# Kernel tuning notes

Hardware: AMD Instinct MI355X
Metric: run time of the kernel (lower is better)

## Reference

```python
import jax, jax.numpy as jnp
import numpy as np

DIM = 512
HEADS = 8
HEAD_DIM = DIM // HEADS
SCALE = HEAD_DIM ** -0.5
LN_EPS = 1e-5


def _layernorm(t, g, b):
    mu = jnp.mean(t, axis=-1, keepdims=True)
    var = jnp.mean(jnp.square(t - mu), axis=-1, keepdims=True)
    return (t - mu) * jax.lax.rsqrt(var + LN_EPS) * g + b


def setup_inputs() -> dict:
    key = jax.random.key(0)
    ks = jax.random.split(key, 8)
    B, C, H, W = 2, DIM, 48, 48
    s = 1.0 / np.sqrt(DIM)
    return {
        "x": jax.random.normal(ks[0], (B, C, H, W), jnp.float32),
        "y": jax.random.normal(ks[1], (B, C, H, W), jnp.float32),
        # linear weights stored [in, out]
        "k_w": jax.random.uniform(ks[2], (DIM, DIM), jnp.float32, -s, s),
        "k_b": jax.random.uniform(ks[3], (DIM,), jnp.float32, -s, s),
        "qv_w": jax.random.uniform(ks[4], (DIM, 2 * DIM), jnp.float32, -s, s),
        "qv_b": jax.random.uniform(ks[5], (2 * DIM,), jnp.float32, -s, s),
        "lnx_g": jnp.ones((DIM,), jnp.float32),
        "lnx_b": jnp.zeros((DIM,), jnp.float32),
        "lny_g": jnp.ones((DIM,), jnp.float32),
        "lny_b": jnp.zeros((DIM,), jnp.float32),
    }


def _split_qv(t, qv_w, qv_b):
    B, N, C = t.shape
    qv = (t @ qv_w + qv_b).reshape(B, N, 2, HEADS, HEAD_DIM)
    qv = jnp.transpose(qv, (2, 0, 3, 1, 4))  # [2, B, h, N, d]
    return qv[0], qv[1]


def _heads(t):
    B, N, C = t.shape
    return jnp.transpose(t.reshape(B, N, HEADS, HEAD_DIM), (0, 2, 1, 3))  # [B,h,N,d]


def reference(x, y, k_w, k_b, qv_w, qv_b, lnx_g, lnx_b, lny_g, lny_b):
    B, C = x.shape[0], x.shape[1]
    xf = _layernorm(jnp.transpose(x.reshape(B, C, -1), (0, 2, 1)), lnx_g, lnx_b)  # [B,N,C]
    yf = _layernorm(jnp.transpose(y.reshape(B, C, -1), (0, 2, 1)), lny_g, lny_b)
    N = xf.shape[1]

    y_q, y_v = _split_qv(yf, qv_w, qv_b)
    x_q, x_v = _split_qv(xf, qv_w, qv_b)
    y_k = _heads(yf @ k_w + k_b)
    x_k = _heads(xf @ k_w + k_b)

    # branch 1: softmax(x_q y_k^T) x_v  -> standard [B,N,C]
    a1 = jax.nn.softmax(jnp.einsum('bhnd,bhmd->bhnm', x_q, y_k) * SCALE, axis=-1)
    xo = jnp.einsum('bhnm,bhmd->bhnd', a1, x_v)
    xo = jnp.transpose(xo, (0, 2, 1, 3)).reshape(B, N, C)

    # branch 2: faithful reproduction of torch quirk (x_k kept a leading 1-dim,
    # so the output [1,B,h,N,d].transpose(1,2).reshape(B,N,C) scrambles layout)
    a2 = jax.nn.softmax(jnp.einsum('bhnd,bhmd->bhnm', y_q, x_k) * SCALE, axis=-1)
    yo = jnp.einsum('bhnm,bhmd->bhnd', a2, y_v)  # [B,h,N,d]
    yo = jnp.transpose(yo[None], (0, 2, 1, 3, 4)).reshape(B, N, C)

    return jnp.concatenate([xo, yo], axis=0)  # [2B, N, C]
```

## Files before the change

### kernel.cpp

```cpp
#include <hip/hip_runtime.h>

#define DIM 512
#define NTOK 2304
#define HEADS 8
#define HD 64
#define LN_EPS 1e-5f
#define BNC 2359296
#define QSC 0.18033688011112042f

typedef __attribute__((ext_vector_type(8))) short short8;
typedef __attribute__((ext_vector_type(4))) short sh4;
typedef __attribute__((ext_vector_type(4))) float f32x4;

__device__ __forceinline__ short f2bf(float f) {
    union { float f; unsigned u; } x; x.f = f;
    unsigned r = (x.u + 0x7fffu + ((x.u >> 16) & 1u)) >> 16;
    return (short)(r & 0xffffu);
}
__device__ __forceinline__ unsigned fbits(float f) {
    union { float f; unsigned u; } x; x.f = f; return x.u;
}
__device__ __forceinline__ void gl2lds(const short* g, short* l) {
    __builtin_amdgcn_global_load_lds(
        (const __attribute__((address_space(1))) unsigned int*)g,
        (__attribute__((address_space(3))) unsigned int*)l, 16, 0, 0);
}

__global__ void k_pre(const float* __restrict__ x, const float* __restrict__ y,
                      const float* __restrict__ qv_w, const float* __restrict__ k_w,
                      const float* __restrict__ qv_b, const float* __restrict__ k_b,
                      const float* __restrict__ gx, const float* __restrict__ bx,
                      const float* __restrict__ gy, const float* __restrict__ by,
                      short* __restrict__ T, short* __restrict__ Wt,
                      float* __restrict__ bias) {
    __shared__ __align__(16) float tile[64][65];
    __shared__ float pS[4][64], pQ[4][64];
    __shared__ float muL[64], rsL[64];
    int bkid = blockIdx.x, tid = threadIdx.x;
    if (bkid < 1152) {
        int nt = bkid % 36, ct = (bkid / 36) % 8, sb = bkid / 288;
        int s = sb >> 1, b = sb & 1;
        int n0 = nt * 64, c0 = ct * 64;
        const float* src = (s ? y : x) + (size_t)b * DIM * NTOK;
        int nl = tid & 63, part = tid >> 6;
        {
            const float* p = src + n0 + nl;
            float sum = 0.f, sq = 0.f;
            for (int c = part * 128; c < part * 128 + 128; c++) {
                float v = p[(size_t)c * NTOK];
                sum += v; sq += v * v;
            }
            pS[part][nl] = sum; pQ[part][nl] = sq;
        }
        __syncthreads();
        if (tid < 64) {
            float ts = pS[0][tid] + pS[1][tid] + pS[2][tid] + pS[3][tid];
            float tq = pQ[0][tid] + pQ[1][tid] + pQ[2][tid] + pQ[3][tid];
            float m = ts * (1.0f / DIM);
            float var = tq * (1.0f / DIM) - m * m;
            muL[tid] = m;
            rsL[tid] = rsqrtf(var + LN_EPS);
        }
        for (int slot = tid; slot < 1024; slot += 256) {
            int r = slot >> 4, q = slot & 15;
            const float* p = src + (size_t)(c0 + r) * NTOK + n0 + q * 4;
            float4 v = *(const float4*)p;
            tile[r][q*4+0] = v.x; tile[r][q*4+1] = v.y;
            tile[r][q*4+2] = v.z; tile[r][q*4+3] = v.w;
        }
        __syncthreads();
        const float* g  = s ? gy : gx;
        const float* be = s ? by : bx;
        int nr = tid >> 2, cg = tid & 3;
        float m = muL[nr], r_ = rsL[nr];
        short8 o0, o1;
        for (int i = 0; i < 8; i++) {
            int c = c0 + cg * 16 + i;
            o0[i] = f2bf((tile[cg*16+i][nr] - m) * r_ * g[c] + be[c]);
        }
        for (int i = 0; i < 8; i++) {
            int c = c0 + cg * 16 + 8 + i;
            o1[i] = f2bf((tile[cg*16+8+i][nr] - m) * r_ * g[c] + be[c]);
        }
        short* dst = T + ((size_t)sb * NTOK + n0 + nr) * DIM + c0 + cg * 16;
        *(short8*)dst = o0;
        *(short8*)(dst + 8) = o1;
        return;
    }
    int idx = bkid - 1152;
    int jt = idx % 24, ct = idx / 24;
    int j0 = jt * 64, c0 = ct * 64;
    if (ct == 0 && tid < 64) {
        int j = j0 + tid;
        bias[j] = (j < 1024) ? qv_b[j] : k_b[j - 1024];
    }
    for (int slot = tid; slot < 1024; slot += 256) {
        int r = slot >> 4, q = slot & 15;
        int c = c0 + r;
        float4 v;
        if (j0 < 1024) v = *(const float4*)(qv_w + (size_t)c * 1024 + j0 + q * 4);
        else           v = *(const float4*)(k_w  + (size_t)c * 512  + (j0 - 1024) + q * 4);
        tile[r][q*4+0] = v.x; tile[r][q*4+1] = v.y;
        tile[r][q*4+2] = v.z; tile[r][q*4+3] = v.w;
    }
    __syncthreads();
    int jr = tid >> 2, cg = tid & 3;
    short8 o0, o1;
    for (int i = 0; i < 8; i++) o0[i] = f2bf(tile[cg*16+i][jr]);
    for (int i = 0; i < 8; i++) o1[i] = f2bf(tile[cg*16+8+i][jr]);
    short* dst = Wt + (size_t)(j0 + jr) * DIM + c0 + cg * 16;
    *(short8*)dst = o0;
    *(short8*)(dst + 8) = o1;
}

__global__ void __launch_bounds__(256)
k_gemm(const short* __restrict__ T, const short* __restrict__ Wt,
       const float* __restrict__ bias, short* __restrict__ QVK,
       short* __restrict__ VT) {
    __shared__ __align__(16) short smem[2 * 128 * 64];
    short* As = smem;
    short* Bs = smem + 128 * 64;
    int n0 = blockIdx.x * 128, j0 = blockIdx.y * 128, sb = blockIdx.z;
    int tid = threadIdx.x;
    int w = tid >> 6, l = tid & 63;
    int wr = w >> 1, wc = w & 1;
    int lrow = l & 15, quad = l >> 4;
    int r_in = (l >> 3) & 7, cc = l & 7;
    int ch = cc ^ r_in;
    int sw0 = (quad ^ (lrow & 7)) * 8;
    const short* Ab = T + (size_t)sb * NTOK * DIM;
    f32x4 acc[4][4] = {};
    for (int kk = 0; kk < 8; kk++) {
        if (kk) __syncthreads();
        for (int inst = 0; inst < 4; inst++) {
            int R = w * 32 + inst * 8 + r_in;
            gl2lds(Ab + (size_t)(n0 + R) * 512 + kk * 64 + ch * 8,
                   &As[(w * 32 + inst * 8) * 64]);
            gl2lds(Wt + (size_t)(j0 + R) * 512 + kk * 64 + ch * 8,
                   &Bs[(w * 32 + inst * 8) * 64]);
        }
        __syncthreads();
        for (int c2 = 0; c2 < 2; c2++) {
            int off = c2 ? (sw0 ^ 32) : sw0;
            short8 af[4], bf[4];
            for (int i = 0; i < 4; i++)
                af[i] = *(const short8*)&As[(wr*64 + i*16 + lrow) * 64 + off];
            for (int j = 0; j < 4; j++)
                bf[j] = *(const short8*)&Bs[(wc*64 + j*16 + lrow) * 64 + off];
            for (int i = 0; i < 4; i++)
                for (int j = 0; j < 4; j++)
                    acc[i][j] = __builtin_amdgcn_mfma_f32_16x16x32_bf16(af[i], bf[j], acc[i][j], 0, 0, 0);
        }
    }
    if (j0 >= 512 && j0 < 1024) {
        __syncthreads();
        for (int i = 0; i < 4; i++)
            for (int j = 0; j < 4; j++) {
                int jloc = wc * 64 + j * 16 + lrow;
                float bv = bias[j0 + jloc];
                int nloc = wr * 64 + i * 16 + quad * 4;
                int c8 = nloc >> 3, half = (nloc >> 2) & 1;
                sh4 pk;
                for (int reg = 0; reg < 4; reg++) pk[reg] = f2bf(acc[i][j][reg] + bv);
                *(sh4*)&smem[jloc * 128 + ((c8 ^ (jloc & 15)) * 8) + half * 4] = pk;
            }
        __syncthreads();
        for (int slot = tid; slot < 2048; slot += 256) {
            int row = slot >> 4, seg = slot & 15;
            short8 v = *(const short8*)&smem[row * 128 + ((seg ^ (row & 15)) * 8)];
            *(short8*)(VT + ((size_t)sb * 512 + (j0 - 512) + row) * NTOK + n0 + seg * 8) = v;
        }
    } else {
        for (int i = 0; i < 4; i++)
            for (int j = 0; j < 4; j++) {
                int jj = j0 + wc * 64 + j * 16 + lrow;
                float bv = bias[jj];
                float sc = (jj < 512) ? QSC : 1.0f;
                for (int reg = 0; reg < 4; reg++) {
                    int n = n0 + wr * 64 + i * 16 + quad * 4 + reg;
                    QVK[((size_t)sb * NTOK + n) * 1536 + jj] = f2bf((acc[i][j][reg] + bv) * sc);
                }
            }
    }
}

__global__ void __launch_bounds__(256)
k_attn(const short* __restrict__ QVK, const short* __restrict__ VT,
       float* __restrict__ out, float* __restrict__ O1,
       float* __restrict__ l0, float* __restrict__ l1) {
    __shared__ __align__(16) short Ks[64 * 64];
    __shared__ __align__(16) short Vs[64 * 64];
    __shared__ __align__(16) short Qs[64 * 64];
    int id = blockIdx.x;
    int half = id / 1152;
    int rid = id % 1152;
    int xcd = rid & 7, rem = rid >> 3;
    int qt = rem % 36, yhi = rem / 36;
    int yb = yhi * 8 + xcd;
    int br = yb >> 4;
    int b  = (yb >> 3) & 1;
    int h  = yb & 7;
    int tid = threadIdx.x;
    int w = tid >> 6, l = tid & 63;
    int lrow = l & 15, quad = l >> 4;
    int r_in = (l >> 3) & 7, cc = l & 7;
    int ch = cc ^ r_in;
    int sw0 = (quad ^ (lrow & 7)) * 8;
    int n0 = qt * 64;
    int m_base = half * 1152;
    const short* Qg = QVK + ((size_t)(br * 2 + b) * NTOK) * 1536 + h * 64;
    const short* Kg = QVK + ((size_t)((1 - br) * 2 + b) * NTOK) * 1536 + 1024 + h * 64;
    const short* Vg = VT + ((size_t)(br * 2 + b) * 512 + h * 64) * NTOK;

    for (int inst = 0; inst < 2; inst++) {
        int R = w * 16 + inst * 8 + r_in;
        gl2lds(Qg + (size_t)(n0 + R) * 1536 + ch * 8, &Qs[(w * 16 + inst * 8) * 64]);
    }

    const short* KgA = Kg + (size_t)(m_base + w * 16 + r_in) * 1536 + ch * 8;
    const short* KgB = Kg + (size_t)(m_base + w * 16 + 8 + r_in) * 1536 + ch * 8;
    const short* VgA = Vg + (size_t)(w * 16 + r_in) * NTOK + m_base + ch * 8;
    const short* VgB = Vg + (size_t)(w * 16 + 8 + r_in) * NTOK + m_base + ch * 8;
    int lds_off = l * 8;

    short8 ka = *(const short8*)(KgA);
    short8 kb = *(const short8*)(KgB);
    short8 va = *(const short8*)(VgA);
    short8 vb = *(const short8*)(VgB);
    const short* Kc = KgA + (size_t)64 * 1536;
    const short* Kd = KgB + (size_t)64 * 1536;
    const short* Vc = VgA + 64;
    const short* Vd = VgB + 64;

    __syncthreads();
    short8 bq0 = *(const short8*)&Qs[(w * 16 + lrow) * 64 + sw0];
    short8 bq1 = *(const short8*)&Qs[(w * 16 + lrow) * 64 + (sw0 ^ 32)];
    short* Pw = &Qs[w * 16 * 64];

    short8 ones;
    for (int i = 0; i < 8; i++) ones[i] = (short)0x3F80;

    f32x4 Oacc[4] = {};
    f32x4 lacc = {};

    for (int mt = 0; mt < 18; mt++) {
        __syncthreads();
        *(short8*)&Ks[(w * 16)     * 64 + lds_off] = ka;
        *(short8*)&Ks[(w * 16 + 8) * 64 + lds_off] = kb;
        *(short8*)&Vs[(w * 16)     * 64 + lds_off] = va;
        *(short8*)&Vs[(w * 16 + 8) * 64 + lds_off] = vb;
        __syncthreads();
        if (mt + 1 < 18) {
            ka = *(const short8*)(Kc);
            kb = *(const short8*)(Kd);
            va = *(const short8*)(Vc);
            vb = *(const short8*)(Vd);
        }
        Kc += (size_t)64 * 1536;
        Kd += (size_t)64 * 1536;
        Vc += 64;
        Vd += 64;
        __builtin_amdgcn_sched_barrier(0);

        for (int sub = 0; sub < 4; sub++) {
            short8 ak0 = *(const short8*)&Ks[(sub * 16 + lrow) * 64 + sw0];
            short8 ak1 = *(const short8*)&Ks[(sub * 16 + lrow) * 64 + (sw0 ^ 32)];
            f32x4 a = {};
            a = __builtin_amdgcn_mfma_f32_16x16x32_bf16(ak0, bq0, a, 0, 0, 0);
            a = __builtin_amdgcn_mfma_f32_16x16x32_bf16(ak1, bq1, a, 0, 0, 0);
            float p0 = exp2f(a[0]), p1 = exp2f(a[1]);
            float p2 = exp2f(a[2]), p3 = exp2f(a[3]);
            uint2 pk;
            pk.x = __builtin_amdgcn_perm(fbits(p1), fbits(p0), 0x07060302u);
            pk.y = __builtin_amdgcn_perm(fbits(p3), fbits(p2), 0x07060302u);
            *(uint2*)&Pw[lrow * 64 + (((2 * sub + (quad >> 1)) ^ (lrow & 7)) * 8) + (quad & 1) * 4] = pk;
        }

        short8 ap0 = *(const short8*)&Pw[lrow * 64 + sw0];
        short8 ap1 = *(const short8*)&Pw[lrow * 64 + (sw0 ^ 32)];
        lacc = __builtin_amdgcn_mfma_f32_16x16x32_bf16(ones, ap0, lacc, 0, 0, 0);
        lacc = __builtin_amdgcn_mfma_f32_16x16x32_bf16(ones, ap1, lacc, 0, 0, 0);
        for (int ddt = 0; ddt < 4; ddt++) {
            short8 av0 = *(const short8*)&Vs[(ddt * 16 + lrow) * 64 + sw0];
            short8 av1 = *(const short8*)&Vs[(ddt * 16 + lrow) * 64 + (sw0 ^ 32)];
            Oacc[ddt] = __builtin_amdgcn_mfma_f32_16x16x32_bf16(av0, ap0, Oacc[ddt], 0, 0, 0);
            Oacc[ddt] = __builtin_amdgcn_mfma_f32_16x16x32_bf16(av1, ap1, Oacc[ddt], 0, 0, 0);
        }
    }

    int n = n0 + w * 16 + lrow;
    if (quad == 0) (half ? l1 : l0)[yb * NTOK + n] = lacc[0];
    for (int ddt = 0; ddt < 4; ddt++) {
        float4 o;
        o.x = Oacc[ddt][0];
        o.y = Oacc[ddt][1];
        o.z = Oacc[ddt][2];
        o.w = Oacc[ddt][3];
        if (half == 0) {
            if (br == 0)
                *(float4*)&out[((size_t)b * NTOK + n) * 512 + h * 64 + ddt * 16 + quad * 4] = o;
            else
                *(float4*)&out[(size_t)BNC + ((size_t)(h * 2 + b) * NTOK + n) * 64 + ddt * 16 + quad * 4] = o;
        } else {
            *(float4*)&O1[((size_t)yb * NTOK + n) * 64 + ddt * 16 + quad * 4] = o;
        }
    }
}

__global__ void __launch_bounds__(256)
k_norm(float* __restrict__ out, const float* __restrict__ O1,
       const float* __restrict__ l0, const float* __restrict__ l1) {
    int i = blockIdx.x * 256 + threadIdx.x;
    int o = i * 4;
    int yb, n, d;
    if (o < BNC) {
        int b = o / (NTOK * 512);
        int r = o % (NTOK * 512);
        n = r >> 9;
        int c = r & 511;
        d = c & 63;
        yb = b * 8 + (c >> 6);
    } else {
        int o2 = o - BNC;
        int hb = o2 / (NTOK * 64);
        n = (o2 >> 6) % NTOK;
        d = o2 & 63;
        yb = 16 + (hb & 1) * 8 + (hb >> 1);
    }
    int li = yb * NTOK + n;
    float linv = 1.f / (l0[li] + l1[li]);
    float4 a = *(const float4*)&out[o];
    float4 q = *(const float4*)&O1[(size_t)li * 64 + d];
    a.x = (a.x + q.x) * linv;
    a.y = (a.y + q.y) * linv;
    a.z = (a.z + q.z) * linv;
    a.w = (a.w + q.w) * linv;
    *(float4*)&out[o] = a;
}

extern "C" void kernel_launch(void* const* d_in, const int* in_sizes, int n_in,
                              void* d_out, int out_size, void* d_ws, size_t ws_size,
                              hipStream_t stream) {
    const float* x     = (const float*)d_in[0];
    const float* y     = (const float*)d_in[1];
    const float* k_w   = (const float*)d_in[2];
    const float* k_b   = (const float*)d_in[3];
    const float* qv_w  = (const float*)d_in[4];
    const float* qv_b  = (const float*)d_in[5];
    const float* lnx_g = (const float*)d_in[6];
    const float* lnx_b = (const float*)d_in[7];
    const float* lny_g = (const float*)d_in[8];
    const float* lny_b = (const float*)d_in[9];
    float* out = (float*)d_out;

    char* ws = (char*)d_ws;
    float* bias = (float*)ws;
    short* T    = (short*)(ws + 6144);
    short* Wt   = T + 4718592;
    short* QVK  = Wt + 786432;
    short* VT   = QVK + 14155776;
    float* O1   = (float*)(ws + 48764928);
    float* l0   = (float*)(ws + 67639296);
    float* l1   = (float*)(ws + 67934208);

    k_pre  <<<1344, 256, 0, stream>>>(x, y, qv_w, k_w, qv_b, k_b,
                                      lnx_g, lnx_b, lny_g, lny_b, T, Wt, bias);
    k_gemm <<<dim3(18, 12, 4), 256, 0, stream>>>(T, Wt, bias, QVK, VT);
    k_attn <<<2304, 256, 0, stream>>>(QVK, VT, out, O1, l0, l1);
    k_norm <<<4608, 256, 0, stream>>>(out, O1, l0, l1);
}
```

Baseline: 202.3 us.

## Double-buffer K/V tiles in LDS and use native exp2 intrinsic

Splits the K and V shared-memory tiles into two buffers so that the next tile is written to LDS after the current tile's MFMA work, leaving one barrier per iteration instead of two. Global loads are issued two tiles ahead in registers. exp2f is also replaced with the hardware exp2 builtin to skip range handling. This costs double the LDS for K/V, which may lower occupancy. The native exp2 may also differ for denormal or edge inputs.

```diff
diff --git a/kernel.cpp b/kernel.cpp
--- a/kernel.cpp
+++ b/kernel.cpp
@@ -188,8 +188,8 @@
 k_attn(const short* __restrict__ QVK, const short* __restrict__ VT,
        float* __restrict__ out, float* __restrict__ O1,
        float* __restrict__ l0, float* __restrict__ l1) {
-    __shared__ __align__(16) short Ks[64 * 64];
-    __shared__ __align__(16) short Vs[64 * 64];
+    __shared__ __align__(16) short Kbuf[2][64 * 64];
+    __shared__ __align__(16) short Vbuf[2][64 * 64];
     __shared__ __align__(16) short Qs[64 * 64];
     int id = blockIdx.x;
     int half = id / 1152;
@@ -217,50 +217,46 @@
         gl2lds(Qg + (size_t)(n0 + R) * 1536 + ch * 8, &Qs[(w * 16 + inst * 8) * 64]);
     }
 
-    const short* KgA = Kg + (size_t)(m_base + w * 16 + r_in) * 1536 + ch * 8;
-    const short* KgB = Kg + (size_t)(m_base + w * 16 + 8 + r_in) * 1536 + ch * 8;
-    const short* VgA = Vg + (size_t)(w * 16 + r_in) * NTOK + m_base + ch * 8;
-    const short* VgB = Vg + (size_t)(w * 16 + 8 + r_in) * NTOK + m_base + ch * 8;
+    const short* KnA = Kg + (size_t)(m_base + w * 16 + r_in) * 1536 + ch * 8;
+    const short* KnB = Kg + (size_t)(m_base + w * 16 + 8 + r_in) * 1536 + ch * 8;
+    const short* VnA = Vg + (size_t)(w * 16 + r_in) * NTOK + m_base + ch * 8;
+    const short* VnB = Vg + (size_t)(w * 16 + 8 + r_in) * NTOK + m_base + ch * 8;
     int lds_off = l * 8;
 
-    short8 ka = *(const short8*)(KgA);
-    short8 kb = *(const short8*)(KgB);
-    short8 va = *(const short8*)(VgA);
-    short8 vb = *(const short8*)(VgB);
-    const short* Kc = KgA + (size_t)64 * 1536;
-    const short* Kd = KgB + (size_t)64 * 1536;
-    const short* Vc = VgA + 64;
-    const short* Vd = VgB + 64;
+    short8 ka = *(const short8*)(KnA);
+    short8 kb = *(const short8*)(KnB);
+    short8 va = *(const short8*)(VnA);
+    short8 vb = *(const short8*)(VnB);
+    KnA += (size_t)64 * 1536; KnB += (size_t)64 * 1536;
+    VnA += 64; VnB += 64;
 
     __syncthreads();
     short8 bq0 = *(const short8*)&Qs[(w * 16 + lrow) * 64 + sw0];
     short8 bq1 = *(const short8*)&Qs[(w * 16 + lrow) * 64 + (sw0 ^ 32)];
     short* Pw = &Qs[w * 16 * 64];
 
+    *(short8*)&Kbuf[0][(w * 16)     * 64 + lds_off] = ka;
+    *(short8*)&Kbuf[0][(w * 16 + 8) * 64 + lds_off] = kb;
+    *(short8*)&Vbuf[0][(w * 16)     * 64 + lds_off] = va;
+    *(short8*)&Vbuf[0][(w * 16 + 8) * 64 + lds_off] = vb;
+    ka = *(const short8*)(KnA);
+    kb = *(const short8*)(KnB);
+    va = *(const short8*)(VnA);
+    vb = *(const short8*)(VnB);
+    KnA += (size_t)64 * 1536; KnB += (size_t)64 * 1536;
+    VnA += 64; VnB += 64;
+
     short8 ones;
     for (int i = 0; i < 8; i++) ones[i] = (short)0x3F80;
 
     f32x4 Oacc[4] = {};
     f32x4 lacc = {};
+    int cur = 0;
 
     for (int mt = 0; mt < 18; mt++) {
         __syncthreads();
-        *(short8*)&Ks[(w * 16)     * 64 + lds_off] = ka;
-        *(short8*)&Ks[(w * 16 + 8) * 64 + lds_off] = kb;
-        *(short8*)&Vs[(w * 16)     * 64 + lds_off] = va;
-        *(short8*)&Vs[(w * 16 + 8) * 64 + lds_off] = vb;
-        __syncthreads();
-        if (mt + 1 < 18) {
-            ka = *(const short8*)(Kc);
-            kb = *(const short8*)(Kd);
-            va = *(const short8*)(Vc);
-            vb = *(const short8*)(Vd);
-        }
-        Kc += (size_t)64 * 1536;
-        Kd += (size_t)64 * 1536;
-        Vc += 64;
-        Vd += 64;
-        __builtin_amdgcn_sched_barrier(0);
+        const short* Ks = Kbuf[cur];
+        const short* Vs = Vbuf[cur];
 
         for (int sub = 0; sub < 4; sub++) {
             short8 ak0 = *(const short8*)&Ks[(sub * 16 + lrow) * 64 + sw0];
@@ -268,8 +264,8 @@
             f32x4 a = {};
             a = __builtin_amdgcn_mfma_f32_16x16x32_bf16(ak0, bq0, a, 0, 0, 0);
             a = __builtin_amdgcn_mfma_f32_16x16x32_bf16(ak1, bq1, a, 0, 0, 0);
-            float p0 = exp2f(a[0]), p1 = exp2f(a[1]);
-            float p2 = exp2f(a[2]), p3 = exp2f(a[3]);
+            float p0 = __builtin_amdgcn_exp2f(a[0]), p1 = __builtin_amdgcn_exp2f(a[1]);
+            float p2 = __builtin_amdgcn_exp2f(a[2]), p3 = __builtin_amdgcn_exp2f(a[3]);
             uint2 pk;
             pk.x = __builtin_amdgcn_perm(fbits(p1), fbits(p0), 0x07060302u);
             pk.y = __builtin_amdgcn_perm(fbits(p3), fbits(p2), 0x07060302u);
@@ -286,6 +282,22 @@
             Oacc[ddt] = __builtin_amdgcn_mfma_f32_16x16x32_bf16(av0, ap0, Oacc[ddt], 0, 0, 0);
             Oacc[ddt] = __builtin_amdgcn_mfma_f32_16x16x32_bf16(av1, ap1, Oacc[ddt], 0, 0, 0);
         }
+
+        if (mt + 1 < 18) {
+            *(short8*)&Kbuf[cur ^ 1][(w * 16)     * 64 + lds_off] = ka;
+            *(short8*)&Kbuf[cur ^ 1][(w * 16 + 8) * 64 + lds_off] = kb;
+            *(short8*)&Vbuf[cur ^ 1][(w * 16)     * 64 + lds_off] = va;
+            *(short8*)&Vbuf[cur ^ 1][(w * 16 + 8) * 64 + lds_off] = vb;
+        }
+        if (mt + 2 < 18) {
+            ka = *(const short8*)(KnA);
+            kb = *(const short8*)(KnB);
+            va = *(const short8*)(VnA);
+            vb = *(const short8*)(VnB);
+        }
+        KnA += (size_t)64 * 1536; KnB += (size_t)64 * 1536;
+        VnA += 64; VnB += 64;
+        cur ^= 1;
     }
 
     int n = n0 + w * 16 + lrow;
```

After: 200.3 us. No clear change (-1.0%).
